# Optimization experiments

Measured on AMD Instinct MI355X. Metric: run time of the kernel, lower is better.

## Reference

```python
import jax, jax.numpy as jnp
import numpy as np

GRID_NY, GRID_NX = 74, 74  # ceil(512/7) per module default formula


def _bspline_basis(u):
    # cubic B-spline pieces, stacked on axis 0 -> (4, H, W)
    u2 = u * u
    u3 = u2 * u
    return jnp.stack([
        (-u3 + 3 * u2 - 3 * u + 1) / 6,
        (3 * u3 - 6 * u2 + 4) / 6,
        (-3 * u3 + 3 * u2 + 3 * u + 1) / 6,
        u3 / 6,
    ], axis=0)


def _forward(input_fmap, theta, ny, nx):
    B, H, W, C = input_fmap.shape
    gx, gy = nx - 3, ny - 3
    sx = W / gx
    sy = W / gy  # NOTE: original code uses W for sy too (faithful)

    xg = jnp.linspace(0.0, W - 1, W)
    yg = jnp.linspace(0.0, H - 1, H)
    xt, yt = jnp.meshgrid(xg, yg)  # (H, W)

    pxf = jnp.floor(xt / sx)
    pyf = jnp.floor(yt / sy)
    u = xt / sx - pxf
    v = yt / sy - pyf
    px = pxf.astype(jnp.int32)
    py = pyf.astype(jnp.int32)

    Bu = _bspline_basis(u)  # (4, H, W), indexed by x-offset a
    Bv = _bspline_basis(v)  # (4, H, W), indexed by y-offset c
    Buv = jnp.einsum('ahw,chw->hwac', Bu, Bv)  # (H, W, 4, 4)

    theta = theta.reshape(B, 2, ny, nx)
    theta_x = theta[:, 0]  # (B, ny, nx)
    theta_y = theta[:, 1]

    offs = jnp.arange(4, dtype=jnp.int32)
    # ts[b,h,w,a,c] = theta[b, py+c, px+a]  (a: x offset, c: y offset)
    iy = py[:, :, None, None] + offs[None, None, None, :]  # (H, W, 1->4 on c)
    ix = px[:, :, None, None] + offs[None, None, :, None]  # (H, W, 4 on a)
    ts_x = theta_x[:, iy, ix]  # (B, H, W, 4, 4)
    ts_y = theta_y[:, iy, ix]

    delta_x = jnp.einsum('hwac,bhwac->bhw', Buv, ts_x)
    delta_y = jnp.einsum('hwac,bhwac->bhw', Buv, ts_y)

    xs = xt[None] + delta_x  # (B, H, W)
    ys = yt[None] + delta_y

    # bilinear sampler
    x0 = jnp.floor(xs).astype(jnp.int32)
    y0 = jnp.floor(ys).astype(jnp.int32)
    x1 = jnp.clip(x0 + 1, 0, W - 1)
    y1 = jnp.clip(y0 + 1, 0, H - 1)
    x0 = jnp.clip(x0, 0, W - 1)
    y0 = jnp.clip(y0, 0, H - 1)

    bidx = jnp.arange(B)[:, None, None]
    Ia = input_fmap[bidx, y0, x0]  # (B, H, W, C)
    Ib = input_fmap[bidx, y1, x0]
    Ic = input_fmap[bidx, y0, x1]
    Id = input_fmap[bidx, y1, x1]

    x0f = x0.astype(jnp.float32)
    x1f = x1.astype(jnp.float32)
    y0f = y0.astype(jnp.float32)
    y1f = y1.astype(jnp.float32)
    wa = ((x1f - xs) * (y1f - ys))[..., None]
    wb = ((x1f - xs) * (ys - y0f))[..., None]
    wc = ((xs - x0f) * (y1f - ys))[..., None]
    wd = ((xs - x0f) * (ys - y0f))[..., None]

    out = wa * Ia + wb * Ib + wc * Ic + wd * Id
    delta = jnp.stack([delta_x, delta_y], axis=0)  # (2, B, H, W)
    return out, delta


def setup_inputs() -> dict:
    key = jax.random.key(0)
    k1, k2 = jax.random.split(key)
    B, H, W, C = 16, 512, 512, 3
    input_fmap = jax.random.normal(k1, (B, H, W, C), dtype=jnp.float32)
    theta = jax.random.normal(k2, (B, 2, GRID_NY, GRID_NX), dtype=jnp.float32)
    return {"input_fmap": input_fmap, "theta": theta, "B": 16}


def reference(input_fmap, theta, B):
    return _forward(input_fmap, theta, GRID_NY, GRID_NX)
```

## Files before the change

kernel.cpp:

```cpp
#include <hip/hip_runtime.h>
#include <math.h>

#define NY 74
#define NX 74
#define HH 512
#define WW 512
#define CC 3
#define BB 16

struct F3 { float a, b, c; };

__global__ __launch_bounds__(256) void stb_kernel(
    const float* __restrict__ fmap, const float* __restrict__ theta,
    float* __restrict__ out, float* __restrict__ delta_out)
{
    const int nwg = BB * HH * 2;
    const int bid = blockIdx.x;
    const int blk = (bid & 7) * (nwg >> 3) + (bid >> 3);

    const int row = blk >> 1;
    const int h = row & (HH - 1);
    const int b = row >> 9;
    const int w0 = (blk & 1) << 8;

    const float inv_s = 71.0f / 512.0f;
    const float c6 = 1.0f / 6.0f;

    __shared__ float2 S[NX];

    const int t = threadIdx.x;
    if (t < NX) {
        float qy = (float)h * inv_s;
        float v = qy - floorf(qy);
        int py = (int)floorf(qy);
        float Bv0 = (((-v + 3.f) * v - 3.f) * v + 1.f) * c6;
        float Bv1 = ((3.f * v - 6.f) * v * v + 4.f) * c6;
        float Bv2 = (((-3.f * v + 3.f) * v + 3.f) * v + 1.f) * c6;
        float Bv3 = (v * v * v) * c6;

        const float* thx = theta + b * 2 * NY * NX;
        const float* thy = thx + NY * NX;
        int base = py * NX + t;
        float sxv = Bv0 * thx[base] + Bv1 * thx[base + NX] +
                    Bv2 * thx[base + 2 * NX] + Bv3 * thx[base + 3 * NX];
        float syv = Bv0 * thy[base] + Bv1 * thy[base + NX] +
                    Bv2 * thy[base + 2 * NX] + Bv3 * thy[base + 3 * NX];
        S[t] = make_float2(sxv, syv);
    }
    __syncthreads();

    const int w = w0 + t;
    const float xw = (float)w;
    const float yh = (float)h;

    float qx = xw * inv_s;
    float u = qx - floorf(qx);
    int px = (int)floorf(qx);
    float Bu0 = (((-u + 3.f) * u - 3.f) * u + 1.f) * c6;
    float Bu1 = ((3.f * u - 6.f) * u * u + 4.f) * c6;
    float Bu2 = (((-3.f * u + 3.f) * u + 3.f) * u + 1.f) * c6;
    float Bu3 = (u * u * u) * c6;

    float2 s0 = S[px], s1 = S[px + 1], s2 = S[px + 2], s3 = S[px + 3];
    float dx = Bu0 * s0.x + Bu1 * s1.x + Bu2 * s2.x + Bu3 * s3.x;
    float dy = Bu0 * s0.y + Bu1 * s1.y + Bu2 * s2.y + Bu3 * s3.y;

    float xs = xw + dx;
    float ys = yh + dy;
    int x0 = (int)floorf(xs);
    int y0 = (int)floorf(ys);
    int x1 = min(max(x0 + 1, 0), WW - 1);
    int y1 = min(max(y0 + 1, 0), HH - 1);
    x0 = min(max(x0, 0), WW - 1);
    y0 = min(max(y0, 0), HH - 1);

    float wa = ((float)x1 - xs) * ((float)y1 - ys);
    float wb = ((float)x1 - xs) * (ys - (float)y0);
    float wc = (xs - (float)x0) * ((float)y1 - ys);
    float wd = (xs - (float)x0) * (ys - (float)y0);

    const float* fb = fmap + b * (HH * WW * CC);
    F3 Ia = *(const F3*)(fb + ((y0 << 9) + x0) * 3);
    F3 Ib = *(const F3*)(fb + ((y1 << 9) + x0) * 3);
    F3 Ic = *(const F3*)(fb + ((y0 << 9) + x1) * 3);
    F3 Id = *(const F3*)(fb + ((y1 << 9) + x1) * 3);

    const int pix = (row << 9) + w;
    float* op = out + pix * 3;
    __builtin_nontemporal_store(wa * Ia.a + wb * Ib.a + wc * Ic.a + wd * Id.a, op + 0);
    __builtin_nontemporal_store(wa * Ia.b + wb * Ib.b + wc * Ic.b + wd * Id.b, op + 1);
    __builtin_nontemporal_store(wa * Ia.c + wb * Ib.c + wc * Ic.c + wd * Id.c, op + 2);

    const int total = BB * HH * WW;
    __builtin_nontemporal_store(dx, delta_out + pix);
    __builtin_nontemporal_store(dy, delta_out + total + pix);
}

extern "C" void kernel_launch(void* const* d_in, const int* in_sizes, int n_in,
                              void* d_out, int out_size, void* d_ws, size_t ws_size,
                              hipStream_t stream) {
    const float* fmap  = (const float*)d_in[0];
    const float* theta = (const float*)d_in[1];
    float* out = (float*)d_out;
    float* delta = out + (size_t)BB * HH * WW * CC;

    dim3 grid(BB * HH * 2), block(256);
    stb_kernel<<<grid, block, 0, stream>>>(fmap, theta, out, delta);
}
```

Measured before the change: 25.56 us.

## Process two pixels per thread with full-row blocks and vectorized stores

```diff
diff --git a/kernel.cpp b/kernel.cpp
--- a/kernel.cpp
+++ b/kernel.cpp
@@ -9,19 +9,22 @@
 #define BB 16
 
 struct F3 { float a, b, c; };
+typedef float v2f __attribute__((ext_vector_type(2)));
+
+__device__ __forceinline__ void nt_store2(float* p, float a, float b) {
+    v2f v; v.x = a; v.y = b;
+    __builtin_nontemporal_store(v, (v2f*)p);
+}
 
 __global__ __launch_bounds__(256) void stb_kernel(
     const float* __restrict__ fmap, const float* __restrict__ theta,
     float* __restrict__ out, float* __restrict__ delta_out)
 {
-    const int nwg = BB * HH * 2;
+    const int nwg = BB * HH;
     const int bid = blockIdx.x;
-    const int blk = (bid & 7) * (nwg >> 3) + (bid >> 3);
-
-    const int row = blk >> 1;
+    const int row = (bid & 7) * (nwg >> 3) + (bid >> 3);
     const int h = row & (HH - 1);
     const int b = row >> 9;
-    const int w0 = (blk & 1) << 8;
 
     const float inv_s = 71.0f / 512.0f;
     const float c6 = 1.0f / 6.0f;
@@ -29,7 +32,9 @@
     __shared__ float2 S[NX];
 
     const int t = threadIdx.x;
-    if (t < NX) {
+    if (t < 2 * NX) {
+        const int comp = (t >= NX) ? 1 : 0;
+        const int j = t - comp * NX;
         float qy = (float)h * inv_s;
         float v = qy - floorf(qy);
         int py = (int)floorf(qy);
@@ -38,62 +43,71 @@
         float Bv2 = (((-3.f * v + 3.f) * v + 3.f) * v + 1.f) * c6;
         float Bv3 = (v * v * v) * c6;
 
-        const float* thx = theta + b * 2 * NY * NX;
-        const float* thy = thx + NY * NX;
-        int base = py * NX + t;
-        float sxv = Bv0 * thx[base] + Bv1 * thx[base + NX] +
-                    Bv2 * thx[base + 2 * NX] + Bv3 * thx[base + 3 * NX];
-        float syv = Bv0 * thy[base] + Bv1 * thy[base + NX] +
-                    Bv2 * thy[base + 2 * NX] + Bv3 * thy[base + 3 * NX];
-        S[t] = make_float2(sxv, syv);
+        const float* th = theta + (b * 2 + comp) * NY * NX;
+        int base = py * NX + j;
+        float s = Bv0 * th[base] + Bv1 * th[base + NX] +
+                  Bv2 * th[base + 2 * NX] + Bv3 * th[base + 3 * NX];
+        ((float*)S)[2 * j + comp] = s;
     }
     __syncthreads();
 
-    const int w = w0 + t;
-    const float xw = (float)w;
     const float yh = (float)h;
+    const float* fb = fmap + b * (HH * WW * CC);
 
-    float qx = xw * inv_s;
-    float u = qx - floorf(qx);
-    int px = (int)floorf(qx);
-    float Bu0 = (((-u + 3.f) * u - 3.f) * u + 1.f) * c6;
-    float Bu1 = ((3.f * u - 6.f) * u * u + 4.f) * c6;
-    float Bu2 = (((-3.f * u + 3.f) * u + 3.f) * u + 1.f) * c6;
-    float Bu3 = (u * u * u) * c6;
+    float o[6], dxy[2][2];
 
-    float2 s0 = S[px], s1 = S[px + 1], s2 = S[px + 2], s3 = S[px + 3];
-    float dx = Bu0 * s0.x + Bu1 * s1.x + Bu2 * s2.x + Bu3 * s3.x;
-    float dy = Bu0 * s0.y + Bu1 * s1.y + Bu2 * s2.y + Bu3 * s3.y;
+    #pragma unroll
+    for (int k = 0; k < 2; ++k) {
+        const int w = 2 * t + k;
+        const float xw = (float)w;
 
-    float xs = xw + dx;
-    float ys = yh + dy;
-    int x0 = (int)floorf(xs);
-    int y0 = (int)floorf(ys);
-    int x1 = min(max(x0 + 1, 0), WW - 1);
-    int y1 = min(max(y0 + 1, 0), HH - 1);
-    x0 = min(max(x0, 0), WW - 1);
-    y0 = min(max(y0, 0), HH - 1);
+        float qx = xw * inv_s;
+        float u = qx - floorf(qx);
+        int px = (int)floorf(qx);
+        float Bu0 = (((-u + 3.f) * u - 3.f) * u + 1.f) * c6;
+        float Bu1 = ((3.f * u - 6.f) * u * u + 4.f) * c6;
+        float Bu2 = (((-3.f * u + 3.f) * u + 3.f) * u + 1.f) * c6;
+        float Bu3 = (u * u * u) * c6;
 
-    float wa = ((float)x1 - xs) * ((float)y1 - ys);
-    float wb = ((float)x1 - xs) * (ys - (float)y0);
-    float wc = (xs - (float)x0) * ((float)y1 - ys);
-    float wd = (xs - (float)x0) * (ys - (float)y0);
+        float2 s0 = S[px], s1 = S[px + 1], s2 = S[px + 2], s3 = S[px + 3];
+        float dx = Bu0 * s0.x + Bu1 * s1.x + Bu2 * s2.x + Bu3 * s3.x;
+        float dy = Bu0 * s0.y + Bu1 * s1.y + Bu2 * s2.y + Bu3 * s3.y;
 
-    const float* fb = fmap + b * (HH * WW * CC);
-    F3 Ia = *(const F3*)(fb + ((y0 << 9) + x0) * 3);
-    F3 Ib = *(const F3*)(fb + ((y1 << 9) + x0) * 3);
-    F3 Ic = *(const F3*)(fb + ((y0 << 9) + x1) * 3);
-    F3 Id = *(const F3*)(fb + ((y1 << 9) + x1) * 3);
+        float xs = xw + dx;
+        float ys = yh + dy;
+        int x0 = (int)floorf(xs);
+        int y0 = (int)floorf(ys);
+        int x1 = min(max(x0 + 1, 0), WW - 1);
+        int y1 = min(max(y0 + 1, 0), HH - 1);
+        x0 = min(max(x0, 0), WW - 1);
+        y0 = min(max(y0, 0), HH - 1);
 
-    const int pix = (row << 9) + w;
+        float wa = ((float)x1 - xs) * ((float)y1 - ys);
+        float wb = ((float)x1 - xs) * (ys - (float)y0);
+        float wc = (xs - (float)x0) * ((float)y1 - ys);
+        float wd = (xs - (float)x0) * (ys - (float)y0);
+
+        F3 Ia = *(const F3*)(fb + ((y0 << 9) + x0) * 3);
+        F3 Ib = *(const F3*)(fb + ((y1 << 9) + x0) * 3);
+        F3 Ic = *(const F3*)(fb + ((y0 << 9) + x1) * 3);
+        F3 Id = *(const F3*)(fb + ((y1 << 9) + x1) * 3);
+
+        o[k * 3 + 0] = wa * Ia.a + wb * Ib.a + wc * Ic.a + wd * Id.a;
+        o[k * 3 + 1] = wa * Ia.b + wb * Ib.b + wc * Ic.b + wd * Id.b;
+        o[k * 3 + 2] = wa * Ia.c + wb * Ib.c + wc * Ic.c + wd * Id.c;
+        dxy[k][0] = dx;
+        dxy[k][1] = dy;
+    }
+
+    const int pix = (row << 9) + 2 * t;
     float* op = out + pix * 3;
-    __builtin_nontemporal_store(wa * Ia.a + wb * Ib.a + wc * Ic.a + wd * Id.a, op + 0);
-    __builtin_nontemporal_store(wa * Ia.b + wb * Ib.b + wc * Ic.b + wd * Id.b, op + 1);
-    __builtin_nontemporal_store(wa * Ia.c + wb * Ib.c + wc * Ic.c + wd * Id.c, op + 2);
+    nt_store2(op + 0, o[0], o[1]);
+    nt_store2(op + 2, o[2], o[3]);
+    nt_store2(op + 4, o[4], o[5]);
 
     const int total = BB * HH * WW;
-    __builtin_nontemporal_store(dx, delta_out + pix);
-    __builtin_nontemporal_store(dy, delta_out + total + pix);
+    nt_store2(delta_out + pix, dxy[0][0], dxy[1][0]);
+    nt_store2(delta_out + total + pix, dxy[0][1], dxy[1][1]);
 }
 
 extern "C" void kernel_launch(void* const* d_in, const int* in_sizes, int n_in,
@@ -104,6 +118,6 @@
     float* out = (float*)d_out;
     float* delta = out + (size_t)BB * HH * WW * CC;
 
-    dim3 grid(BB * HH * 2), block(256);
+    dim3 grid(BB * HH), block(256);
     stb_kernel<<<grid, block, 0, stream>>>(fmap, theta, out, delta);
 }
```

After: 27.80 us. 8.7% more time.
